# Optimization experiments

Measured on AMD Instinct MI355X. Metric: run time of the kernel, lower is better.

Reference implementation:

```python
import jax, jax.numpy as jnp
import numpy as np

N = 4096
D_IMG = 512
D_FEAT = 512
D_H = 256
D_Z = 128
N_CLS = 64
CHANGE_FRAC = 1.0  # alpha


def setup_inputs() -> dict:
    key = jax.random.key(0)
    ks = jax.random.split(key, 12)
    u = jax.random.uniform(ks[0], (N, N))
    a = (jnp.triu(u, 1) < 0.01).astype(jnp.float32)
    adj_ori = a + a.T
    i = jnp.arange(N)
    # GCN-normalized adjacency D^-1/2 (A+I) D^-1/2 (input to ep_net)
    a_hat = adj_ori.at[i, i].set(1.0)
    d = jnp.power(a_hat.sum(1), -0.5)
    adj_norm = a_hat * d[:, None] * d[None, :]
    xav = lambda k, s: jax.random.uniform(k, s, jnp.float32, -1.0, 1.0) * jnp.sqrt(6.0 / (s[0] + s[1]))
    return {
        "adj_norm": adj_norm,
        "adj_ori": adj_ori,
        "feats_ori": jax.random.normal(ks[1], (N, D_FEAT), jnp.float32),
        "img_feats": jax.random.normal(ks[2], (N, D_IMG), jnp.float32),
        "csd_ori": jax.random.normal(ks[3], (N_CLS, D_FEAT), jnp.float32),
        "csd_img": jax.random.normal(ks[4], (N_CLS, D_IMG), jnp.float32),
        "noise": jax.random.normal(ks[5], (N, D_Z), jnp.float32),
        "Wb": xav(ks[6], (D_IMG, D_H)),
        "Wm": xav(ks[7], (D_H, D_Z)),
        "Wl": xav(ks[8], (D_H, D_Z)),
        "fc1_W": xav(ks[9], (2 * D_FEAT, D_H)),
        "fc1_b": jnp.zeros((D_H,), jnp.float32),
        "fc2_W": xav(ks[10], (2 * D_H, D_IMG)),
        "fc2_b": jnp.zeros((D_IMG,), jnp.float32),
    }


def _ceil_st(x):
    # CeilNoGradient: ceil forward, identity backward (straight-through)
    return x + jax.lax.stop_gradient(jnp.ceil(x) - x)


def _gsage_layer(adj, h, W, b, relu):
    neigh = adj @ h
    mean_neigh = neigh / (adj.sum(axis=1, keepdims=True) + 1e-7)
    x = jnp.concatenate((h, mean_neigh), axis=1) @ W + b
    return jax.nn.relu(x) if relu else x


def _sample_adj_edge(adj_logits, adj):
    n_edges = jnp.sum(adj != 0)
    n_change = jnp.floor(n_edges.astype(jnp.float32) * CHANGE_FRAC / 2.0).astype(jnp.int32)
    ep = jnp.triu(adj_logits, 1)
    ep = ep - jnp.min(ep)
    ep = ep / jnp.max(ep)
    T = N * N
    # --- remove lowest-prob existing edges ---
    mask_rm = ep * adj
    v = jnp.sort(mask_rm.reshape(-1))  # ascending; positives at the tail
    n_nz = jnp.sum(v > 0)
    n_rm = jnp.minimum(n_nz, n_change)
    thresh_rm = v[T - n_nz + n_rm - 1]  # n_rm-th smallest positive
    mask_rm = jnp.where(mask_rm > thresh_rm, 0.0, mask_rm)
    mask_rm = _ceil_st(mask_rm)
    mask_rm = mask_rm + mask_rm.T
    adj_new = adj - mask_rm
    # --- add highest-prob missing edges ---
    mask_add = ep * (1.0 - adj)
    v2 = jnp.sort(mask_add.reshape(-1))
    n_nz2 = jnp.sum(v2 > 0)
    n_add = jnp.minimum(n_nz2, n_change)
    thresh_add = v2[T - n_add]  # n_add-th largest positive
    mask_add = jnp.where(mask_add < thresh_add, 0.0, mask_add)
    mask_add = _ceil_st(mask_add)
    mask_add = mask_add + mask_add.T
    return adj_new + mask_add


def reference(adj_norm, adj_ori, feats_ori, img_feats, csd_ori, csd_img, noise,
              Wb, Wm, Wl, fc1_W, fc1_b, fc2_W, fc2_b):
    # ep_net (VGAE, gae=False)
    hidden = adj_norm @ (img_feats @ Wb)
    mean = jax.nn.relu(adj_norm @ (hidden @ Wm))
    logstd = jax.nn.relu(adj_norm @ (hidden @ Wl))
    Z = noise * jnp.exp(logstd) + mean
    adj_logits = Z @ Z.T
    # edge rewiring
    adj_new = _sample_adj_edge(adj_logits, adj_ori)
    # normalize_adj for 'gsage': fill diag 1, L1 row-normalize
    i = jnp.arange(N)
    adj_new = adj_new.at[i, i].set(1.0)
    adj_new = adj_new / jnp.maximum(jnp.sum(jnp.abs(adj_new), axis=1, keepdims=True), 1e-12)
    # nc_net (DGPN)
    preds_img = img_feats @ csd_img.T
    h1 = _gsage_layer(adj_new, feats_ori, fc1_W, fc1_b, relu=True)
    h2 = _gsage_layer(adj_new, h1, fc2_W, fc2_b, relu=False)
    feat_total = jax.nn.log_softmax(h2, axis=-1)
    preds_total = feat_total @ csd_img.T
    return preds_total, feat_total, preds_img, adj_logits
```

## Files before the change

### kernel.cpp

```cpp
#include <hip/hip_runtime.h>
#include <type_traits>
#include <stdint.h>

#define NN 4096
#define TTOT 16777216UL

enum { F_RELU=1, F_ACC=2, F_RS=4, F_BIAS=8 };

typedef unsigned short ushort_t;
using bf16x8 = __attribute__((ext_vector_type(8))) short;
using f32x4  = __attribute__((ext_vector_type(4))) float;

struct SelParams {
  unsigned min_ord, max_ord, n_up;
  float lo, M, c0;
  unsigned n_change, rm_prefix, rm_k, add_prefix, add_k;
  float t_rm, t_add;
  unsigned hist_rm[256], hist_add[256];
};

__device__ __forceinline__ unsigned ordenc(float x){
  unsigned u = __float_as_uint(x);
  return (u & 0x80000000u) ? ~u : (u | 0x80000000u);
}
__device__ __forceinline__ float orddec_ok(unsigned o){
  unsigned u = (o & 0x80000000u) ? (o ^ 0x80000000u) : ~o;
  return __uint_as_float(u);
}
__device__ __forceinline__ ushort_t f2bf(float x){
  unsigned u = __float_as_uint(x);
  return (ushort_t)((u + 0x7FFFu + ((u >> 16) & 1u)) >> 16);
}
__device__ __forceinline__ float bf2f(ushort_t h){
  return __uint_as_float(((unsigned)h) << 16);
}

template<int DN>
__global__ __launch_bounds__(256)
void k_b3t(const float* __restrict__ Bsrc, ushort_t* __restrict__ H,
           ushort_t* __restrict__ Mg, ushort_t* __restrict__ L)
{
  __shared__ ushort_t sh[64][65], sm[64][65], sl[64][65];
  const int t = threadIdx.x;
  const int n0 = blockIdx.x * 64, k0 = blockIdx.y * 64;
  #pragma unroll
  for (int it = 0; it < 16; ++it){
    int idx = it*256 + t; int r = idx >> 6, c = idx & 63;
    float x  = Bsrc[(size_t)(k0 + r)*DN + n0 + c];
    ushort_t hb = f2bf(x);
    float r1 = x - bf2f(hb);
    ushort_t mb = f2bf(r1);
    float r2 = r1 - bf2f(mb);
    ushort_t lb = f2bf(r2);
    sh[r][c] = hb; sm[r][c] = mb; sl[r][c] = lb;
  }
  __syncthreads();
  #pragma unroll
  for (int it = 0; it < 16; ++it){
    int idx = it*256 + t; int r = idx >> 6, c = idx & 63;
    size_t o = (size_t)(n0 + r)*4096 + k0 + c;
    H[o] = sh[c][r]; Mg[o] = sm[c][r]; L[o] = sl[c][r];
  }
}

__global__ __launch_bounds__(256)
void k_mfma(const signed char* __restrict__ A8,
            const ushort_t* __restrict__ BH, const ushort_t* __restrict__ BM2,
            const ushort_t* __restrict__ BL,
            float* __restrict__ C0, float* __restrict__ C1, int N)
{
  __shared__ ushort_t Ab[64][72];
  __shared__ ushort_t Bb[3][64][72];
  const int t = threadIdx.x;
  const int m0 = blockIdx.y * 64, n0 = blockIdx.x * 64;
  const int kz = blockIdx.z;
  const int kbase = kz * 2048;
  float* C = kz ? C1 : C0;
  const int sr = t >> 2, sc = (t & 3) * 16;
  const int w = t >> 6, lane = t & 63;
  const int fr = lane & 15, fg = lane >> 4;

  int4 a_r = *reinterpret_cast<const int4*>(A8 + (size_t)(m0+sr)*4096 + kbase + sc);
  const ushort_t* bsrc0 = BH  + (size_t)(n0+sr)*4096 + kbase + sc;
  const ushort_t* bsrc1 = BM2 + (size_t)(n0+sr)*4096 + kbase + sc;
  const ushort_t* bsrc2 = BL  + (size_t)(n0+sr)*4096 + kbase + sc;
  int4 b0a = reinterpret_cast<const int4*>(bsrc0)[0], b0b = reinterpret_cast<const int4*>(bsrc0)[1];
  int4 b1a = reinterpret_cast<const int4*>(bsrc1)[0], b1b = reinterpret_cast<const int4*>(bsrc1)[1];
  int4 b2a = reinterpret_cast<const int4*>(bsrc2)[0], b2b = reinterpret_cast<const int4*>(bsrc2)[1];

  f32x4 acc[4][3];
  #pragma unroll
  for (int c = 0; c < 4; ++c)
    #pragma unroll
    for (int p = 0; p < 3; ++p)
      acc[c][p] = (f32x4){0.f, 0.f, 0.f, 0.f};

  for (int k0 = 0; k0 < 2048; k0 += 64){
    {
      alignas(16) ushort_t tmp[16];
      const signed char* ab = reinterpret_cast<const signed char*>(&a_r);
      #pragma unroll
      for (int i = 0; i < 16; ++i) tmp[i] = f2bf((float)(int)ab[i]);
      *reinterpret_cast<int4*>(&Ab[sr][sc])     = reinterpret_cast<int4*>(tmp)[0];
      *reinterpret_cast<int4*>(&Ab[sr][sc + 8]) = reinterpret_cast<int4*>(tmp)[1];
      *reinterpret_cast<int4*>(&Bb[0][sr][sc])     = b0a;
      *reinterpret_cast<int4*>(&Bb[0][sr][sc + 8]) = b0b;
      *reinterpret_cast<int4*>(&Bb[1][sr][sc])     = b1a;
      *reinterpret_cast<int4*>(&Bb[1][sr][sc + 8]) = b1b;
      *reinterpret_cast<int4*>(&Bb[2][sr][sc])     = b2a;
      *reinterpret_cast<int4*>(&Bb[2][sr][sc + 8]) = b2b;
    }
    __syncthreads();
    if (k0 + 64 < 2048){
      a_r = *reinterpret_cast<const int4*>(A8 + (size_t)(m0+sr)*4096 + kbase + (k0+64) + sc);
      const ushort_t* p0 = BH  + (size_t)(n0+sr)*4096 + kbase + (k0+64) + sc;
      const ushort_t* p1 = BM2 + (size_t)(n0+sr)*4096 + kbase + (k0+64) + sc;
      const ushort_t* p2 = BL  + (size_t)(n0+sr)*4096 + kbase + (k0+64) + sc;
      b0a = reinterpret_cast<const int4*>(p0)[0]; b0b = reinterpret_cast<const int4*>(p0)[1];
      b1a = reinterpret_cast<const int4*>(p1)[0]; b1b = reinterpret_cast<const int4*>(p1)[1];
      b2a = reinterpret_cast<const int4*>(p2)[0]; b2b = reinterpret_cast<const int4*>(p2)[1];
    }
    #pragma unroll
    for (int kk = 0; kk < 64; kk += 32){
      bf16x8 af = *reinterpret_cast<const bf16x8*>(&Ab[w*16 + fr][kk + fg*8]);
      #pragma unroll
      for (int c = 0; c < 4; ++c){
        const int bn = c*16 + fr;
        bf16x8 bh = *reinterpret_cast<const bf16x8*>(&Bb[0][bn][kk + fg*8]);
        acc[c][0] = __builtin_amdgcn_mfma_f32_16x16x32_bf16(af, bh, acc[c][0], 0, 0, 0);
        bf16x8 bm = *reinterpret_cast<const bf16x8*>(&Bb[1][bn][kk + fg*8]);
        acc[c][1] = __builtin_amdgcn_mfma_f32_16x16x32_bf16(af, bm, acc[c][1], 0, 0, 0);
        bf16x8 bl = *reinterpret_cast<const bf16x8*>(&Bb[2][bn][kk + fg*8]);
        acc[c][2] = __builtin_amdgcn_mfma_f32_16x16x32_bf16(af, bl, acc[c][2], 0, 0, 0);
      }
    }
    __syncthreads();
  }
  #pragma unroll
  for (int c = 0; c < 4; ++c){
    f32x4 s = acc[c][0] + acc[c][1];
    s = s + acc[c][2];
    #pragma unroll
    for (int r = 0; r < 4; ++r)
      C[(size_t)(m0 + w*16 + fg*4 + r)*N + n0 + c*16 + fr] = s[r];
  }
}

__global__ __launch_bounds__(256)
void k_add2(const float* __restrict__ A, const float* __restrict__ B,
            float* __restrict__ O, int n4)
{
  int i = blockIdx.x*256 + threadIdx.x;
  if (i < n4){
    float4 a = reinterpret_cast<const float4*>(A)[i];
    float4 b = reinterpret_cast<const float4*>(B)[i];
    reinterpret_cast<float4*>(O)[i] = make_float4(a.x+b.x, a.y+b.y, a.z+b.z, a.w+b.w);
  }
}

template<typename TA>
__global__ __launch_bounds__(256)
void k_gemm32(const TA* __restrict__ A, const float* __restrict__ B,
              float* __restrict__ C, int M, int N, int K, int ldc,
              const float* __restrict__ rowscale, const float* __restrict__ bias,
              int flags)
{
  __shared__ float As[16][36];
  __shared__ float Bs[16][68];
  const int t  = threadIdx.x;
  const int tx = t & 15, ty = t >> 4;
  const int m0 = blockIdx.y * 32, n0 = blockIdx.x * 64;
  float acc[2][4] = {};
  for (int k0 = 0; k0 < K; k0 += 16) {
    if (t < 128){
      const int mA = t >> 2, kA = (t & 3) * 4;
      if constexpr (std::is_same<TA, float>::value) {
        float4 v = *reinterpret_cast<const float4*>(A + (size_t)(m0+mA)*K + (k0+kA));
        As[kA+0][mA]=v.x; As[kA+1][mA]=v.y; As[kA+2][mA]=v.z; As[kA+3][mA]=v.w;
      } else {
        int u = *reinterpret_cast<const int*>(A + (size_t)(m0+mA)*K + (k0+kA));
        As[kA+0][mA]=(float)(int)(signed char)( u       & 0xff);
        As[kA+1][mA]=(float)(int)(signed char)((u>>8)   & 0xff);
        As[kA+2][mA]=(float)(int)(signed char)((u>>16)  & 0xff);
        As[kA+3][mA]=(float)(int)(signed char)((u>>24)  & 0xff);
      }
    }
    {
      const int kB = t >> 4, nB = (t & 15) * 4;
      float4 w = *reinterpret_cast<const float4*>(B + (size_t)(k0+kB)*N + (n0+nB));
      Bs[kB][nB+0]=w.x; Bs[kB][nB+1]=w.y; Bs[kB][nB+2]=w.z; Bs[kB][nB+3]=w.w;
    }
    __syncthreads();
    #pragma unroll
    for (int kk = 0; kk < 16; ++kk) {
      float a0 = As[kk][ty*2+0];
      float a1 = As[kk][ty*2+1];
      float4 bv = *reinterpret_cast<const float4*>(&Bs[kk][tx*4]);
      float b[4]={bv.x,bv.y,bv.z,bv.w};
      #pragma unroll
      for (int j=0;j<4;++j){
        acc[0][j] = fmaf(a0, b[j], acc[0][j]);
        acc[1][j] = fmaf(a1, b[j], acc[1][j]);
      }
    }
    __syncthreads();
  }
  #pragma unroll
  for (int i=0;i<2;++i){
    const int m = m0 + ty*2 + i;
    const float rsv = (flags & F_RS) ? rowscale[m] : 1.0f;
    float* cp = C + (size_t)m*ldc + (n0 + tx*4);
    float o[4];
    #pragma unroll
    for (int j=0;j<4;++j){
      float v = acc[i][j] * rsv;
      if (flags & F_BIAS) v += bias[n0 + tx*4 + j];
      if (flags & F_ACC)  v += cp[j];
      if (flags & F_RELU) v = fmaxf(v, 0.0f);
      o[j] = v;
    }
    *reinterpret_cast<float4*>(cp) = make_float4(o[0],o[1],o[2],o[3]);
  }
}

__global__ __launch_bounds__(256)
void k_gemm32T(const float* __restrict__ A, const float* __restrict__ B,
               float* __restrict__ C, int M, int N, int K, int ldc)
{
  __shared__ float As[16][36];
  __shared__ float Bs[16][68];
  const int t  = threadIdx.x;
  const int tx = t & 15, ty = t >> 4;
  const int m0 = blockIdx.y * 32, n0 = blockIdx.x * 64;
  float acc[2][4] = {};
  for (int k0 = 0; k0 < K; k0 += 16) {
    if (t < 128){
      const int mA = t >> 2, kA = (t & 3) * 4;
      float4 v = *reinterpret_cast<const float4*>(A + (size_t)(m0+mA)*K + (k0+kA));
      As[kA+0][mA]=v.x; As[kA+1][mA]=v.y; As[kA+2][mA]=v.z; As[kA+3][mA]=v.w;
    }
    {
      const int nB = t >> 2, kB = (t & 3) * 4;
      float4 w = *reinterpret_cast<const float4*>(B + (size_t)(n0+nB)*K + (k0+kB));
      Bs[kB+0][nB]=w.x; Bs[kB+1][nB]=w.y; Bs[kB+2][nB]=w.z; Bs[kB+3][nB]=w.w;
    }
    __syncthreads();
    #pragma unroll
    for (int kk = 0; kk < 16; ++kk) {
      float a0 = As[kk][ty*2+0];
      float a1 = As[kk][ty*2+1];
      float4 bv = *reinterpret_cast<const float4*>(&Bs[kk][tx*4]);
      float b[4]={bv.x,bv.y,bv.z,bv.w};
      #pragma unroll
      for (int j=0;j<4;++j){
        acc[0][j] = fmaf(a0, b[j], acc[0][j]);
        acc[1][j] = fmaf(a1, b[j], acc[1][j]);
      }
    }
    __syncthreads();
  }
  #pragma unroll
  for (int i=0;i<2;++i){
    const int m = m0 + ty*2 + i;
    float* cp = C + (size_t)m*ldc + (n0 + tx*4);
    *reinterpret_cast<float4*>(cp) = make_float4(acc[i][0],acc[i][1],acc[i][2],acc[i][3]);
  }
}

__global__ __launch_bounds__(256)
void k_fc(const float* __restrict__ A1, const float* __restrict__ B1,
          const float* __restrict__ bias,
          const float* __restrict__ A2, const float* __restrict__ B2,
          const float* __restrict__ rowscale,
          float* __restrict__ C, int N, int K1, int K2, int relu)
{
  __shared__ float As[16][36];
  __shared__ float Bs[16][68];
  const int t  = threadIdx.x;
  const int tx = t & 15, ty = t >> 4;
  const int m0 = blockIdx.y * 32, n0 = blockIdx.x * 64;
  float acc1[2][4] = {};
  float acc2[2][4] = {};
  for (int k0 = 0; k0 < K1; k0 += 16) {
    if (t < 128){
      const int mA = t >> 2, kA = (t & 3) * 4;
      float4 v = *reinterpret_cast<const float4*>(A1 + (size_t)(m0+mA)*K1 + (k0+kA));
      As[kA+0][mA]=v.x; As[kA+1][mA]=v.y; As[kA+2][mA]=v.z; As[kA+3][mA]=v.w;
    }
    {
      const int kB = t >> 4, nB = (t & 15) * 4;
      float4 w = *reinterpret_cast<const float4*>(B1 + (size_t)(k0+kB)*N + (n0+nB));
      Bs[kB][nB+0]=w.x; Bs[kB][nB+1]=w.y; Bs[kB][nB+2]=w.z; Bs[kB][nB+3]=w.w;
    }
    __syncthreads();
    #pragma unroll
    for (int kk = 0; kk < 16; ++kk) {
      float a0 = As[kk][ty*2+0];
      float a1 = As[kk][ty*2+1];
      float4 bv = *reinterpret_cast<const float4*>(&Bs[kk][tx*4]);
      float b[4]={bv.x,bv.y,bv.z,bv.w};
      #pragma unroll
      for (int j=0;j<4;++j){
        acc1[0][j] = fmaf(a0, b[j], acc1[0][j]);
        acc1[1][j] = fmaf(a1, b[j], acc1[1][j]);
      }
    }
    __syncthreads();
  }
  for (int k0 = 0; k0 < K2; k0 += 16) {
    if (t < 128){
      const int mA = t >> 2, kA = (t & 3) * 4;
      float4 v = *reinterpret_cast<const float4*>(A2 + (size_t)(m0+mA)*K2 + (k0+kA));
      As[kA+0][mA]=v.x; As[kA+1][mA]=v.y; As[kA+2][mA]=v.z; As[kA+3][mA]=v.w;
    }
    {
      const int kB = t >> 4, nB = (t & 15) * 4;
      float4 w = *reinterpret_cast<const float4*>(B2 + (size_t)(k0+kB)*N + (n0+nB));
      Bs[kB][nB+0]=w.x; Bs[kB][nB+1]=w.y; Bs[kB][nB+2]=w.z; Bs[kB][nB+3]=w.w;
    }
    __syncthreads();
    #pragma unroll
    for (int kk = 0; kk < 16; ++kk) {
      float a0 = As[kk][ty*2+0];
      float a1 = As[kk][ty*2+1];
      float4 bv = *reinterpret_cast<const float4*>(&Bs[kk][tx*4]);
      float b[4]={bv.x,bv.y,bv.z,bv.w};
      #pragma unroll
      for (int j=0;j<4;++j){
        acc2[0][j] = fmaf(a0, b[j], acc2[0][j]);
        acc2[1][j] = fmaf(a1, b[j], acc2[1][j]);
      }
    }
    __syncthreads();
  }
  #pragma unroll
  for (int i=0;i<2;++i){
    const int m = m0 + ty*2 + i;
    const float rsv = rowscale[m];
    float* cp = C + (size_t)m*N + (n0 + tx*4);
    float o[4];
    #pragma unroll
    for (int j=0;j<4;++j){
      float t1 = acc1[i][j] + bias[n0 + tx*4 + j];
      float v  = acc2[i][j] * rsv;
      v += t1;
      if (relu) v = fmaxf(v, 0.0f);
      o[j] = v;
    }
    *reinterpret_cast<float4*>(cp) = make_float4(o[0],o[1],o[2],o[3]);
  }
}

__global__ __launch_bounds__(256)
void k_wcat(const float* __restrict__ Wm, const float* __restrict__ Wl,
            float* __restrict__ Wcat)
{
  int idx = blockIdx.x*256 + threadIdx.x;
  int row = idx >> 8, col = idx & 255;
  Wcat[idx] = (col < 128) ? Wm[row*128 + col] : Wl[row*128 + (col - 128)];
}

template<int D>
__global__ __launch_bounds__(256)
void k_spmmF(const float* __restrict__ A, const float* __restrict__ B,
             float* __restrict__ C)
{
  const int row = blockIdx.x, t = threadIdx.x;
  const int lane = t & 63, wv = t >> 6;
  __shared__ int   sc[288];
  __shared__ float sv[288];
  __shared__ int wtot[4];
  __shared__ int nsh;
  const float4* r4 = reinterpret_cast<const float4*>(A + (size_t)row*NN) + t*4;
  float lv[16];
  #pragma unroll
  for (int q=0;q<4;++q){
    float4 v = r4[q];
    lv[q*4+0]=v.x; lv[q*4+1]=v.y; lv[q*4+2]=v.z; lv[q*4+3]=v.w;
  }
  int c = 0;
  #pragma unroll
  for (int k=0;k<16;++k) c += (lv[k] != 0.0f);
  int inc = c;
  #pragma unroll
  for (int off=1; off<64; off<<=1){
    int v = __shfl_up(inc, off, 64);
    if (lane >= off) inc += v;
  }
  if (lane == 63) wtot[wv] = inc;
  __syncthreads();
  int wbase = 0;
  #pragma unroll
  for (int ww=0; ww<3; ++ww) if (ww < wv) wbase += wtot[ww];
  int pos = wbase + inc - c;
  #pragma unroll
  for (int k=0;k<16;++k){
    if (lv[k] != 0.0f){
      if (pos >= 0 && pos < 288){ sc[pos] = t*16+k; sv[pos] = lv[k]; }
      pos++;
    }
  }
  if (t == 255){
    int tot = wbase + inc;
    nsh = (tot < 288) ? tot : 288;
  }
  __syncthreads();
  const int n = nsh;
  float acc = 0.f;
  int s = 0;
  for (; s+4 <= n; s += 4){
    float x0 = B[(size_t)sc[s+0]*D + t];
    float x1 = B[(size_t)sc[s+1]*D + t];
    float x2 = B[(size_t)sc[s+2]*D + t];
    float x3 = B[(size_t)sc[s+3]*D + t];
    acc = fmaf(sv[s+0], x0, acc);
    acc = fmaf(sv[s+1], x1, acc);
    acc = fmaf(sv[s+2], x2, acc);
    acc = fmaf(sv[s+3], x3, acc);
  }
  for (; s < n; ++s) acc = fmaf(sv[s], B[(size_t)sc[s]*D + t], acc);
  C[(size_t)row*D + t] = acc;
}

__global__ __launch_bounds__(256)
void k_zzt(const float* __restrict__ Z, float* __restrict__ C)
{
  const int bx = blockIdx.x, by = blockIdx.y;
  if (by > bx) return;
  __shared__ float As[16][68];
  __shared__ float Bs[16][68];
  const int t = threadIdx.x, tx = t & 15, ty = t >> 4;
  const int m0 = by*64, n0 = bx*64;
  const int mA = t >> 2, kA = (t & 3) * 4;
  float acc[4][4] = {};
  for (int k0 = 0; k0 < 128; k0 += 16){
    float4 va = *reinterpret_cast<const float4*>(Z + (size_t)(m0+mA)*128 + k0 + kA);
    As[kA+0][mA]=va.x; As[kA+1][mA]=va.y; As[kA+2][mA]=va.z; As[kA+3][mA]=va.w;
    float4 vb = *reinterpret_cast<const float4*>(Z + (size_t)(n0+mA)*128 + k0 + kA);
    Bs[kA+0][mA]=vb.x; Bs[kA+1][mA]=vb.y; Bs[kA+2][mA]=vb.z; Bs[kA+3][mA]=vb.w;
    __syncthreads();
    #pragma unroll
    for (int kk = 0; kk < 16; ++kk) {
      float4 av = *reinterpret_cast<const float4*>(&As[kk][ty*4]);
      float4 bv = *reinterpret_cast<const float4*>(&Bs[kk][tx*4]);
      float a[4]={av.x,av.y,av.z,av.w};
      float b[4]={bv.x,bv.y,bv.z,bv.w};
      #pragma unroll
      for (int i=0;i<4;++i)
        #pragma unroll
        for (int j=0;j<4;++j)
          acc[i][j] = fmaf(a[i], b[j], acc[i][j]);
    }
    __syncthreads();
  }
  #pragma unroll
  for (int i=0;i<4;++i){
    float* cp = C + (size_t)(m0+ty*4+i)*NN + (n0 + tx*4);
    *reinterpret_cast<float4*>(cp) = make_float4(acc[i][0],acc[i][1],acc[i][2],acc[i][3]);
  }
  if (bx != by){
    for (int c0 = 0; c0 < 64; c0 += 16){
      __syncthreads();
      if (tx >= c0/4 && tx < c0/4 + 4){
        #pragma unroll
        for (int i=0;i<4;++i)
          #pragma unroll
          for (int j=0;j<4;++j)
            As[tx*4 + j - c0][ty*4 + i] = acc[i][j];
      }
      __syncthreads();
      const int c = t & 63, r0 = t >> 6;
      #pragma unroll
      for (int rr = 0; rr < 4; ++rr)
        C[(size_t)(n0 + c0 + r0 + rr*4)*NN + m0 + c] = As[r0 + rr*4][c];
    }
  }
}

__global__ __launch_bounds__(256)
void k_z2(const float* __restrict__ MPLP, const float* __restrict__ noise,
          float* __restrict__ Z)
{
  int i = blockIdx.x*256 + threadIdx.x;
  int m = i >> 7, c = i & 127;
  float mp = fmaxf(MPLP[(size_t)m*256 + c], 0.0f);
  float lp = fmaxf(MPLP[(size_t)m*256 + 128 + c], 0.0f);
  Z[i] = noise[i]*expf(lp) + mp;
}

__global__ __launch_bounds__(256)
void k_initstats(SelParams* p)
{
  int t = threadIdx.x;
  if (t == 0){
    p->min_ord = 0xFFFFFFFFu; p->max_ord = 0u; p->n_up = 0u;
    p->rm_prefix = 0u; p->add_prefix = 0u;
  }
  p->hist_rm[t] = 0u; p->hist_add[t] = 0u;
}

__global__ __launch_bounds__(256)
void k_stats1(const float* __restrict__ L, const float* __restrict__ adj,
              unsigned long long* __restrict__ mask, SelParams* __restrict__ p)
{
  unsigned mn=0xFFFFFFFFu, mx=0u, cnt=0u;
  size_t g = (size_t)blockIdx.x*256 + threadIdx.x;
  const size_t stride = (size_t)gridDim.x*256;
  for (; g < 262144; g += stride){
    const int i  = (int)(g >> 6);
    const int jb = (int)(g & 63) << 6;
    unsigned long long m = 0ull;
    if (jb + 63 > i){
      const float4* a4 = reinterpret_cast<const float4*>(adj + (size_t)i*NN + jb);
      const float4* l4 = reinterpret_cast<const float4*>(L   + (size_t)i*NN + jb);
      for (int w = 0; w < 16; ++w){
        const int j0 = jb + w*4;
        if (j0 + 3 <= i) continue;
        float4 av = a4[w]; float4 lv = l4[w];
        float ae[4]={av.x,av.y,av.z,av.w};
        float le[4]={lv.x,lv.y,lv.z,lv.w};
        #pragma unroll
        for (int e=0;e<4;++e){
          const int jj = j0 + e;
          if (jj > i){
            if (ae[e] != 0.0f){ m |= 1ull << (jj & 63); cnt++; }
            unsigned o = ordenc(le[e]);
            mn = (o < mn) ? o : mn;
            mx = (o > mx) ? o : mx;
          }
        }
      }
    }
    mask[g] = m;
  }
  __shared__ unsigned smn[256], smx[256], sc[256];
  int t = threadIdx.x;
  smn[t]=mn; smx[t]=mx; sc[t]=cnt; __syncthreads();
  for (int s=128; s>0; s>>=1){
    if (t < s){
      smn[t] = (smn[t+s] < smn[t]) ? smn[t+s] : smn[t];
      smx[t] = (smx[t+s] > smx[t]) ? smx[t+s] : smx[t];
      sc[t] += sc[t+s];
    }
    __syncthreads();
  }
  if (t == 0){
    atomicMin(&p->min_ord, smn[0]);
    atomicMax(&p->max_ord, smx[0]);
    atomicAdd(&p->n_up, sc[0]);
  }
}

__global__ void k_stats2(SelParams* p)
{
  float mnv = orddec_ok(p->min_ord), mxv = orddec_ok(p->max_ord);
  float lo = fminf(mnv, 0.0f), hi = fmaxf(mxv, 0.0f);
  p->lo = lo;
  p->M  = hi - lo;
  p->c0 = (0.0f - lo) / p->M;
  p->n_change = p->n_up;
}

__global__ __launch_bounds__(256)
void k_hist2(const float* __restrict__ L, const unsigned long long* __restrict__ mask,
             SelParams* __restrict__ p, int shift)
{
  __shared__ unsigned hr[256], ha[256];
  const int t = threadIdx.x;
  hr[t]=0u; ha[t]=0u; __syncthreads();
  const float lo = p->lo, Mv = p->M;
  const unsigned pr = p->rm_prefix, pa = p->add_prefix;
  const float4* L4 = reinterpret_cast<const float4*>(L);
  size_t q = (size_t)blockIdx.x*256 + t;
  const size_t stride = (size_t)gridDim.x*256;
  for (; q < TTOT/4; q += stride){
    const int i = (int)(q >> 10);
    const int j = (int)(q & 1023) << 2;
    if (j + 3 <= i) continue;
    float4 l = L4[q];
    const unsigned long long w = mask[q >> 4];
    float le[4]={l.x,l.y,l.z,l.w};
    #pragma unroll
    for (int e=0;e<4;++e){
      const int jj = j + e;
      if (jj <= i) continue;
      const unsigned key = __float_as_uint((le[e] - lo) / Mv);
      if (key == 0u) continue;
      const bool edge = (w >> (jj & 63)) & 1ull;
      if (edge){
        if (shift == 24 || (key >> (shift+8)) == pr) atomicAdd(&hr[(key>>shift)&255u], 1u);
      } else {
        if (shift == 24 || (key >> (shift+8)) == pa) atomicAdd(&ha[(key>>shift)&255u], 1u);
      }
    }
  }
  __syncthreads();
  if (hr[t]) atomicAdd(&p->hist_rm[t], hr[t]);
  if (ha[t]) atomicAdd(&p->hist_add[t], ha[t]);
}

__global__ __launch_bounds__(256)
void k_scan2(SelParams* __restrict__ p, int shift)
{
  const int t = threadIdx.x;
  if (t == 0){
    const unsigned c0k  = __float_as_uint(p->c0);
    const unsigned n_up = p->n_up;
    {
      unsigned injb = 300u, inj = 0u;
      if (c0k != 0u && (shift == 24 || (c0k >> (shift+8)) == p->rm_prefix)){
        injb = (c0k >> shift) & 255u; inj = n_up;
      }
      unsigned k;
      if (shift == 24){
        unsigned tot = inj;
        for (int d=0; d<256; ++d) tot += p->hist_rm[d];
        k = (tot < p->n_change) ? tot : p->n_change;
      } else k = p->rm_k;
      unsigned cum = 0u, digit = 255u;
      for (int d=0; d<256; ++d){
        unsigned hd = p->hist_rm[d] + (((unsigned)d == injb) ? inj : 0u);
        if (cum + hd >= k){ digit = (unsigned)d; k -= cum; break; }
        cum += hd;
      }
      p->rm_prefix = (p->rm_prefix << 8) | digit;
      p->rm_k = k;
      if (shift == 0) p->t_rm = __uint_as_float(p->rm_prefix);
    }
    {
      unsigned injb = 300u, inj = 0u;
      if (c0k != 0u && (shift == 24 || (c0k >> (shift+8)) == p->add_prefix)){
        injb = (c0k >> shift) & 255u;
        inj  = 8386560u - n_up + 4096u;
      }
      unsigned k;
      if (shift == 24){
        unsigned tot = inj;
        for (int d=0; d<256; ++d) tot += p->hist_add[d];
        k = (tot < p->n_change) ? tot : p->n_change;
      } else k = p->add_k;
      unsigned cum = 0u, digit = 0u;
      for (int d=255; d>=0; --d){
        unsigned hd = p->hist_add[d] + (((unsigned)d == injb) ? inj : 0u);
        if (cum + hd >= k){ digit = (unsigned)d; k -= cum; break; }
        cum += hd;
      }
      p->add_prefix = (p->add_prefix << 8) | digit;
      p->add_k = k;
      if (shift == 0) p->t_add = __uint_as_float(p->add_prefix);
    }
  }
  __syncthreads();
  p->hist_rm[t] = 0u; p->hist_add[t] = 0u;
}

__device__ __forceinline__ int adjval(bool edge, float v, float c0v, float trm, float tad)
{
  int rmU = (edge && v   >  0.0f && v   <= trm) ? 1 : 0;
  int rmL = (edge && c0v >  0.0f && c0v <= trm) ? 1 : 0;
  int adU = (!edge && v   >= tad) ? 1 : 0;
  int adL = (!edge && c0v >= tad) ? 1 : 0;
  return (edge ? 1 : 0) - rmU - rmL + adU + adL;
}

__global__ __launch_bounds__(256)
void k_apply(const float* __restrict__ L, const unsigned long long* __restrict__ mask,
             const SelParams* __restrict__ p, signed char* __restrict__ A8)
{
  const int bx = blockIdx.x, by = blockIdx.y;
  if (by > bx) return;
  const float lo=p->lo, Mv=p->M, c0v=p->c0, trm=p->t_rm, tad=p->t_add;
  const int i0 = by*64, j0 = bx*64, t = threadIdx.x;
  __shared__ signed char Vs[64][65];
  if (bx == by){
    for (int it=0; it<16; ++it){
      int e = it*256 + t; int r = e>>6, c = e&63;
      size_t idx = (size_t)(i0+r)*NN + (j0+c);
      if (r < c){
        bool edge = (mask[idx>>6] >> ((j0+c) & 63)) & 1ull;
        float v = (L[idx] - lo) / Mv;
        int val = adjval(edge, v, c0v, trm, tad);
        A8[idx] = (signed char)val;
        Vs[c][r] = (signed char)val;
      } else if (r == c){
        A8[idx] = 1;
      }
    }
    __syncthreads();
    for (int it=0; it<16; ++it){
      int e = it*256 + t; int r = e>>6, c = e&63;
      if (r > c) A8[(size_t)(i0+r)*NN + (j0+c)] = Vs[r][c];
    }
  } else {
    for (int it=0; it<16; ++it){
      int e = it*256 + t; int r = e>>6, c = e&63;
      size_t idx = (size_t)(i0+r)*NN + (j0+c);
      bool edge = (mask[idx>>6] >> ((j0+c) & 63)) & 1ull;
      float v = (L[idx] - lo) / Mv;
      int val = adjval(edge, v, c0v, trm, tad);
      A8[idx] = (signed char)val;
      Vs[c][r] = (signed char)val;
    }
    __syncthreads();
    for (int it=0; it<16; ++it){
      int e = it*256 + t; int r = e>>6, c = e&63;
      A8[(size_t)(j0+r)*NN + (i0+c)] = Vs[r][c];
    }
  }
}

__global__ __launch_bounds__(256)
void k_rowsum8(const signed char* __restrict__ A8, float* __restrict__ s_mean)
{
  const int row = blockIdx.x, t = threadIdx.x;
  const int4 w = reinterpret_cast<const int4*>(A8 + (size_t)row*NN)[t];
  int s = 0, a = 0;
  int vs[4] = {w.x, w.y, w.z, w.w};
  #pragma unroll
  for (int q=0; q<4; ++q){
    int u = vs[q];
    #pragma unroll
    for (int b=0; b<4; ++b){
      int c = (int)(signed char)((u >> (8*b)) & 0xff);
      s += c; a += (c < 0) ? -c : c;
    }
  }
  __shared__ int rs_[256], ra_[256];
  rs_[t]=s; ra_[t]=a; __syncthreads();
  for (int st=128; st>0; st>>=1){
    if (t < st){ rs_[t]+=rs_[t+st]; ra_[t]+=ra_[t+st]; }
    __syncthreads();
  }
  if (t == 0){
    float rs = (float)rs_[0], ra = (float)ra_[0];
    float A = fmaxf(ra, 1e-12f);
    s_mean[row] = (1.0f / A) / (rs / A + 1e-7f);
  }
}

__global__ __launch_bounds__(256)
void k_lsm(float* __restrict__ X)
{
  const int row = blockIdx.x, t = threadIdx.x;
  float* x = X + (size_t)row*512;
  float v0 = x[t], v1 = x[t+256];
  __shared__ float red[256];
  red[t] = fmaxf(v0, v1); __syncthreads();
  for (int s=128; s>0; s>>=1){
    if (t < s) red[t] = fmaxf(red[t], red[t+s]);
    __syncthreads();
  }
  float m = red[0]; __syncthreads();
  red[t] = expf(v0-m) + expf(v1-m); __syncthreads();
  for (int s=128; s>0; s>>=1){
    if (t < s) red[t] += red[t+s];
    __syncthreads();
  }
  float ls = logf(red[0]);
  x[t]     = (v0 - m) - ls;
  x[t+256] = (v1 - m) - ls;
}

extern "C" void kernel_launch(void* const* d_in, const int* in_sizes, int n_in,
                              void* d_out, int out_size, void* d_ws, size_t ws_size,
                              hipStream_t stream)
{
  (void)in_sizes; (void)n_in; (void)out_size; (void)ws_size;
  const float* adj_norm = (const float*)d_in[0];
  const float* adj_ori  = (const float*)d_in[1];
  const float* feats    = (const float*)d_in[2];
  const float* img      = (const float*)d_in[3];
  const float* csd_img  = (const float*)d_in[5];
  const float* noise    = (const float*)d_in[6];
  const float* Wb       = (const float*)d_in[7];
  const float* Wm       = (const float*)d_in[8];
  const float* Wl       = (const float*)d_in[9];
  const float* fc1W     = (const float*)d_in[10];
  const float* fc1b     = (const float*)d_in[11];
  const float* fc2W     = (const float*)d_in[12];
  const float* fc2b     = (const float*)d_in[13];

  float* out    = (float*)d_out;
  float* out_pt = out;
  float* out_ft = out + 262144;
  float* out_pi = out + 2359296;
  float* out_lg = out + 2621440;

  char* W = (char*)d_ws;
  signed char* adj8 = (signed char*)W;
  float* bufA   = (float*)(W + (16u<<20));
  float* bufB   = (float*)(W + (24u<<20));
  float* HMHL   = (float*)(W + (28u<<20));
  float* MPLP   = (float*)(W + (32u<<20));
  float* Z      = (float*)(W + (36u<<20));
  unsigned long long* mask = (unsigned long long*)(W + (38u<<20));
  float* p2q0   = (float*)(W + (40u<<20));
  float* s_mean = (float*)(W + (44u<<20));
  SelParams* sp = (SelParams*)(W + (44u<<20) + 65536);
  float* Wcat   = (float*)(W + (45u<<20));
  ushort_t* BT1h = (ushort_t*)(W + (28u<<20));
  ushort_t* BT1m = (ushort_t*)(W + (32u<<20));
  ushort_t* BT1l = (ushort_t*)(W + (36u<<20));
  ushort_t* BT2h = (ushort_t*)(W + (28u<<20));
  ushort_t* BT2m = (ushort_t*)(W + (30u<<20));
  ushort_t* BT2l = (ushort_t*)(W + (32u<<20));

  dim3 B(256);
  auto G32 = [](int M, int N){ return dim3((unsigned)(N/64), (unsigned)(M/32)); };

  k_gemm32<float><<<G32(4096,256),B,0,stream>>>(img, Wb, bufA, 4096,256,512,256, nullptr,nullptr,0);
  k_spmmF<256><<<4096,B,0,stream>>>(adj_norm, bufA, bufB);
  k_wcat<<<256,B,0,stream>>>(Wm, Wl, Wcat);
  k_gemm32<float><<<G32(4096,256),B,0,stream>>>(bufB, Wcat, HMHL, 4096,256,256,256, nullptr,nullptr,0);
  k_spmmF<256><<<4096,B,0,stream>>>(adj_norm, HMHL, MPLP);
  k_z2<<<2048,B,0,stream>>>(MPLP, noise, Z);
  k_zzt<<<dim3(64,64),B,0,stream>>>(Z, out_lg);

  k_initstats<<<1,B,0,stream>>>(sp);
  k_stats1<<<1024,B,0,stream>>>(out_lg, adj_ori, mask, sp);
  k_stats2<<<1,1,0,stream>>>(sp);
  for (int shift = 24; shift >= 0; shift -= 8){
    k_hist2<<<2048,B,0,stream>>>(out_lg, mask, sp, shift);
    k_scan2<<<1,B,0,stream>>>(sp, shift);
  }
  k_apply<<<dim3(64,64),B,0,stream>>>(out_lg, mask, sp, adj8);

  k_rowsum8<<<4096,B,0,stream>>>(adj8, s_mean);

  k_b3t<512><<<dim3(8,64),B,0,stream>>>(feats, BT1h, BT1m, BT1l);
  k_mfma<<<dim3(8,64,2),B,0,stream>>>(adj8, BT1h, BT1m, BT1l, bufA, out_ft, 512);
  k_add2<<<2048,B,0,stream>>>(bufA, out_ft, bufA, 524288);
  k_fc<<<G32(4096,256),B,0,stream>>>(feats, fc1W, fc1b, bufA, fc1W + 512*256, s_mean,
                                     bufB, 256, 512, 512, 1);
  k_b3t<256><<<dim3(4,64),B,0,stream>>>(bufB, BT2h, BT2m, BT2l);
  k_mfma<<<dim3(4,64,2),B,0,stream>>>(adj8, BT2h, BT2m, BT2l, p2q0, out_ft, 256);
  k_add2<<<1024,B,0,stream>>>(p2q0, out_ft, bufA, 262144);
  k_fc<<<G32(4096,512),B,0,stream>>>(bufB, fc2W, fc2b, bufA, fc2W + 256*512, s_mean,
                                     out_ft, 512, 256, 256, 0);
  k_lsm<<<4096,B,0,stream>>>(out_ft);

  k_gemm32T<<<G32(4096,64),B,0,stream>>>(out_ft, csd_img, out_pt, 4096,64,512,64);
  k_gemm32T<<<G32(4096,64),B,0,stream>>>(img, csd_img, out_pi, 4096,64,512,64);
}
```

Measured before the change: 834.0 us.

## Compute Z·Zᵀ with bf16x3 split MFMA instead of fp32 FMA tiles

Fuses a three-way bf16 split (high/mid/low) into the Z construction kernel. The scalar fp32 shared-memory Z·Zᵀ kernel is replaced with an MFMA kernel that runs six bf16 products per tile to approximate fp32 accuracy. The symmetric mirror write now goes through an LDS staging tile using float4 stores. The goal is to move the 4096x4096x128 product onto the matrix cores, at the cost of six times the MFMA work and operands loaded straight from global memory without LDS reuse.

```diff
diff --git a/kernel.cpp b/kernel.cpp
--- a/kernel.cpp
+++ b/kernel.cpp
@@ -155,6 +155,82 @@
     float4 a = reinterpret_cast<const float4*>(A)[i];
     float4 b = reinterpret_cast<const float4*>(B)[i];
     reinterpret_cast<float4*>(O)[i] = make_float4(a.x+b.x, a.y+b.y, a.z+b.z, a.w+b.w);
+  }
+}
+
+__global__ __launch_bounds__(256)
+void k_z2p(const float* __restrict__ MPLP, const float* __restrict__ noise,
+           ushort_t* __restrict__ ZH, ushort_t* __restrict__ ZM,
+           ushort_t* __restrict__ ZL)
+{
+  int i = blockIdx.x*256 + threadIdx.x;
+  int m = i >> 7, c = i & 127;
+  float mp = fmaxf(MPLP[(size_t)m*256 + c], 0.0f);
+  float lp = fmaxf(MPLP[(size_t)m*256 + 128 + c], 0.0f);
+  float z = noise[i]*expf(lp) + mp;
+  ushort_t hb = f2bf(z);
+  float r1 = z - bf2f(hb);
+  ushort_t mb = f2bf(r1);
+  float r2 = r1 - bf2f(mb);
+  ushort_t lb = f2bf(r2);
+  ZH[i] = hb; ZM[i] = mb; ZL[i] = lb;
+}
+
+__global__ __launch_bounds__(256)
+void k_zztm(const ushort_t* __restrict__ ZH, const ushort_t* __restrict__ ZM,
+            const ushort_t* __restrict__ ZL, float* __restrict__ C)
+{
+  const int bx = blockIdx.x, by = blockIdx.y;
+  if (by > bx) return;
+  __shared__ float Cs[64][68];
+  const int t = threadIdx.x;
+  const int m0 = by*64, n0 = bx*64;
+  const int w = t >> 6, lane = t & 63;
+  const int fr = lane & 15, fg = lane >> 4;
+  const int arow = m0 + w*16 + fr;
+
+  f32x4 acc[4];
+  #pragma unroll
+  for (int c = 0; c < 4; ++c) acc[c] = (f32x4){0.f,0.f,0.f,0.f};
+
+  #pragma unroll
+  for (int kk = 0; kk < 128; kk += 32){
+    bf16x8 ah = *reinterpret_cast<const bf16x8*>(ZH + (size_t)arow*128 + kk + fg*8);
+    bf16x8 am = *reinterpret_cast<const bf16x8*>(ZM + (size_t)arow*128 + kk + fg*8);
+    bf16x8 al = *reinterpret_cast<const bf16x8*>(ZL + (size_t)arow*128 + kk + fg*8);
+    #pragma unroll
+    for (int c = 0; c < 4; ++c){
+      const int brow = n0 + c*16 + fr;
+      bf16x8 bh = *reinterpret_cast<const bf16x8*>(ZH + (size_t)brow*128 + kk + fg*8);
+      bf16x8 bm = *reinterpret_cast<const bf16x8*>(ZM + (size_t)brow*128 + kk + fg*8);
+      bf16x8 bl = *reinterpret_cast<const bf16x8*>(ZL + (size_t)brow*128 + kk + fg*8);
+      acc[c] = __builtin_amdgcn_mfma_f32_16x16x32_bf16(ah, bh, acc[c], 0, 0, 0);
+      acc[c] = __builtin_amdgcn_mfma_f32_16x16x32_bf16(ah, bm, acc[c], 0, 0, 0);
+      acc[c] = __builtin_amdgcn_mfma_f32_16x16x32_bf16(am, bh, acc[c], 0, 0, 0);
+      acc[c] = __builtin_amdgcn_mfma_f32_16x16x32_bf16(ah, bl, acc[c], 0, 0, 0);
+      acc[c] = __builtin_amdgcn_mfma_f32_16x16x32_bf16(al, bh, acc[c], 0, 0, 0);
+      acc[c] = __builtin_amdgcn_mfma_f32_16x16x32_bf16(am, bm, acc[c], 0, 0, 0);
+    }
+  }
+  #pragma unroll
+  for (int c = 0; c < 4; ++c)
+    #pragma unroll
+    for (int r = 0; r < 4; ++r)
+      Cs[w*16 + fg*4 + r][c*16 + fr] = acc[c][r];
+  __syncthreads();
+  const int rr = t >> 2, cb = (t & 3) * 16;
+  #pragma unroll
+  for (int j = 0; j < 4; ++j){
+    float4 v = *reinterpret_cast<const float4*>(&Cs[rr][cb + j*4]);
+    *reinterpret_cast<float4*>(&C[(size_t)(m0+rr)*NN + n0 + cb + j*4]) = v;
+  }
+  if (bx != by){
+    #pragma unroll
+    for (int j = 0; j < 4; ++j){
+      float4 v = make_float4(Cs[cb+j*4+0][rr], Cs[cb+j*4+1][rr],
+                             Cs[cb+j*4+2][rr], Cs[cb+j*4+3][rr]);
+      *reinterpret_cast<float4*>(&C[(size_t)(n0+rr)*NN + m0 + cb + j*4]) = v;
+    }
   }
 }
 
@@ -420,72 +496,6 @@
   }
   for (; s < n; ++s) acc = fmaf(sv[s], B[(size_t)sc[s]*D + t], acc);
   C[(size_t)row*D + t] = acc;
-}
-
-__global__ __launch_bounds__(256)
-void k_zzt(const float* __restrict__ Z, float* __restrict__ C)
-{
-  const int bx = blockIdx.x, by = blockIdx.y;
-  if (by > bx) return;
-  __shared__ float As[16][68];
-  __shared__ float Bs[16][68];
-  const int t = threadIdx.x, tx = t & 15, ty = t >> 4;
-  const int m0 = by*64, n0 = bx*64;
-  const int mA = t >> 2, kA = (t & 3) * 4;
-  float acc[4][4] = {};
-  for (int k0 = 0; k0 < 128; k0 += 16){
-    float4 va = *reinterpret_cast<const float4*>(Z + (size_t)(m0+mA)*128 + k0 + kA);
-    As[kA+0][mA]=va.x; As[kA+1][mA]=va.y; As[kA+2][mA]=va.z; As[kA+3][mA]=va.w;
-    float4 vb = *reinterpret_cast<const float4*>(Z + (size_t)(n0+mA)*128 + k0 + kA);
-    Bs[kA+0][mA]=vb.x; Bs[kA+1][mA]=vb.y; Bs[kA+2][mA]=vb.z; Bs[kA+3][mA]=vb.w;
-    __syncthreads();
-    #pragma unroll
-    for (int kk = 0; kk < 16; ++kk) {
-      float4 av = *reinterpret_cast<const float4*>(&As[kk][ty*4]);
-      float4 bv = *reinterpret_cast<const float4*>(&Bs[kk][tx*4]);
-      float a[4]={av.x,av.y,av.z,av.w};
-      float b[4]={bv.x,bv.y,bv.z,bv.w};
-      #pragma unroll
-      for (int i=0;i<4;++i)
-        #pragma unroll
-        for (int j=0;j<4;++j)
-          acc[i][j] = fmaf(a[i], b[j], acc[i][j]);
-    }
-    __syncthreads();
-  }
-  #pragma unroll
-  for (int i=0;i<4;++i){
-    float* cp = C + (size_t)(m0+ty*4+i)*NN + (n0 + tx*4);
-    *reinterpret_cast<float4*>(cp) = make_float4(acc[i][0],acc[i][1],acc[i][2],acc[i][3]);
-  }
-  if (bx != by){
-    for (int c0 = 0; c0 < 64; c0 += 16){
-      __syncthreads();
-      if (tx >= c0/4 && tx < c0/4 + 4){
-        #pragma unroll
-        for (int i=0;i<4;++i)
-          #pragma unroll
-          for (int j=0;j<4;++j)
-            As[tx*4 + j - c0][ty*4 + i] = acc[i][j];
-      }
-      __syncthreads();
-      const int c = t & 63, r0 = t >> 6;
-      #pragma unroll
-      for (int rr = 0; rr < 4; ++rr)
-        C[(size_t)(n0 + c0 + r0 + rr*4)*NN + m0 + c] = As[r0 + rr*4][c];
-    }
-  }
-}
-
-__global__ __launch_bounds__(256)
-void k_z2(const float* __restrict__ MPLP, const float* __restrict__ noise,
-          float* __restrict__ Z)
-{
-  int i = blockIdx.x*256 + threadIdx.x;
-  int m = i >> 7, c = i & 127;
-  float mp = fmaxf(MPLP[(size_t)m*256 + c], 0.0f);
-  float lp = fmaxf(MPLP[(size_t)m*256 + 128 + c], 0.0f);
-  Z[i] = noise[i]*expf(lp) + mp;
 }
 
 __global__ __launch_bounds__(256)
@@ -792,12 +802,14 @@
   float* bufB   = (float*)(W + (24u<<20));
   float* HMHL   = (float*)(W + (28u<<20));
   float* MPLP   = (float*)(W + (32u<<20));
-  float* Z      = (float*)(W + (36u<<20));
   unsigned long long* mask = (unsigned long long*)(W + (38u<<20));
   float* p2q0   = (float*)(W + (40u<<20));
   float* s_mean = (float*)(W + (44u<<20));
   SelParams* sp = (SelParams*)(W + (44u<<20) + 65536);
   float* Wcat   = (float*)(W + (45u<<20));
+  ushort_t* ZH = (ushort_t*)(W + (40u<<20));
+  ushort_t* ZM = (ushort_t*)(W + (41u<<20));
+  ushort_t* ZL = (ushort_t*)(W + (42u<<20));
   ushort_t* BT1h = (ushort_t*)(W + (28u<<20));
   ushort_t* BT1m = (ushort_t*)(W + (32u<<20));
   ushort_t* BT1l = (ushort_t*)(W + (36u<<20));
@@ -813,8 +825,8 @@
   k_wcat<<<256,B,0,stream>>>(Wm, Wl, Wcat);
   k_gemm32<float><<<G32(4096,256),B,0,stream>>>(bufB, Wcat, HMHL, 4096,256,256,256, nullptr,nullptr,0);
   k_spmmF<256><<<4096,B,0,stream>>>(adj_norm, HMHL, MPLP);
-  k_z2<<<2048,B,0,stream>>>(MPLP, noise, Z);
-  k_zzt<<<dim3(64,64),B,0,stream>>>(Z, out_lg);
+  k_z2p<<<2048,B,0,stream>>>(MPLP, noise, ZH, ZM, ZL);
+  k_zztm<<<dim3(64,64),B,0,stream>>>(ZH, ZM, ZL, out_lg);
 
   k_initstats<<<1,B,0,stream>>>(sp);
   k_stats1<<<1024,B,0,stream>>>(out_lg, adj_ori, mask, sp);
```

Result: slower. 906.1 us (+8.6%).
